# Kernel optimization log

Measured on AMD Instinct MI355X. Metric: run time of the kernel, lower is better.

Reference implementation:

```python
import jax, jax.numpy as jnp
import numpy as np

N_NODES = 50000
N_EDGES = 800000
NUM_FEATURES = 96
HIDDEN = 96


def _glorot(key, fan_in, fan_out):
    s = np.sqrt(6.0 / (fan_in + fan_out)).astype(np.float32)
    return jax.random.uniform(key, (fan_in, fan_out), minval=-s, maxval=s, dtype=jnp.float32)


def setup_inputs() -> dict:
    key = jax.random.key(0)
    ks = jax.random.split(key, 8)
    x = jax.random.normal(ks[0], (N_NODES, NUM_FEATURES), dtype=jnp.float32)
    edge_index = jax.random.randint(ks[1], (2, N_EDGES), 0, N_NODES, dtype=jnp.int64)
    return {
        "x": x,
        "W1": _glorot(ks[2], NUM_FEATURES, HIDDEN),
        "b1": jnp.zeros((HIDDEN,), jnp.float32),
        "W2": _glorot(ks[3], HIDDEN, HIDDEN),
        "b2": jnp.zeros((HIDDEN,), jnp.float32),
        "W3": _glorot(ks[4], HIDDEN, HIDDEN),
        "b3": jnp.zeros((HIDDEN,), jnp.float32),
        "edge_index": edge_index,
    }


def _gcn_conv(x, src, dst, W, b):
    """PyG GCNConv: add self-loops, symmetric normalization D^-1/2 (A+I) D^-1/2 X W + b."""
    n = x.shape[0]
    h = x @ W  # [N, H]
    # degree with self-loops (in-degree over dst, +1 for the self-loop)
    deg = jax.ops.segment_sum(jnp.ones_like(dst, dtype=h.dtype), dst, num_segments=n) + 1.0
    dinv = jax.lax.rsqrt(deg)  # [N]
    norm = dinv[src] * dinv[dst]  # [E]
    # scatter normalized messages; self-loop contributes h_i / deg_i
    agg = jax.ops.segment_sum(h[src] * norm[:, None], dst, num_segments=n)
    return agg + h * (dinv * dinv)[:, None] + b


def reference(x, W1, b1, W2, b2, W3, b3, edge_index):
    src, dst = edge_index[0], edge_index[1]
    # dropout is a no-op in eval mode (F.dropout with training=False)
    h = jax.nn.relu(_gcn_conv(x, src, dst, W1, b1))
    h = jax.nn.relu(_gcn_conv(h, src, dst, W2, b2))
    return _gcn_conv(h, src, dst, W3, b3)
```

## Files before the change

### kernel.cpp

```cpp
#include <hip/hip_runtime.h>

#define F 96
#define SCAN_B 1024
#define CHUNKS 8
#define CW 12
#define EWIN 2048

#define WT_IDX(c, k) ((c) * 96 + (((k) ^ (((c) & 7) << 2))))


__global__ void k_zero_i(int* __restrict__ p, int n) {
    int i = blockIdx.x * blockDim.x + threadIdx.x;
    if (i < n) p[i] = 0;
}

__global__ void k_hist(const int* __restrict__ dst, int* __restrict__ hist, int E) {
    int e = blockIdx.x * blockDim.x + threadIdx.x;
    if (e < E) atomicAdd(&hist[dst[e]], 1);
}

__global__ void k_dinv(const int* __restrict__ hist, float* __restrict__ dinv, int N) {
    int i = blockIdx.x * blockDim.x + threadIdx.x;
    if (i < N) dinv[i] = rsqrtf((float)hist[i] + 1.0f);
}

__global__ __launch_bounds__(SCAN_B) void k_scan1(const int* __restrict__ hist,
                                                  int* __restrict__ incl,
                                                  int* __restrict__ bsum, int N) {
    __shared__ int s[SCAN_B];
    int i = blockIdx.x * SCAN_B + threadIdx.x;
    int v = (i < N) ? hist[i] : 0;
    s[threadIdx.x] = v;
    __syncthreads();
    for (int off = 1; off < SCAN_B; off <<= 1) {
        int add = (threadIdx.x >= off) ? s[threadIdx.x - off] : 0;
        __syncthreads();
        s[threadIdx.x] += add;
        __syncthreads();
    }
    if (i < N) incl[i] = s[threadIdx.x];
    if (threadIdx.x == SCAN_B - 1) bsum[blockIdx.x] = s[SCAN_B - 1];
}

__global__ __launch_bounds__(SCAN_B) void k_scan2(int* __restrict__ bsum, int nb) {
    __shared__ int s[SCAN_B];
    int v = (threadIdx.x < nb) ? bsum[threadIdx.x] : 0;
    s[threadIdx.x] = v;
    __syncthreads();
    for (int off = 1; off < SCAN_B; off <<= 1) {
        int add = (threadIdx.x >= off) ? s[threadIdx.x - off] : 0;
        __syncthreads();
        s[threadIdx.x] += add;
        __syncthreads();
    }
    if (threadIdx.x < nb) bsum[threadIdx.x] = s[threadIdx.x] - v;
}

__global__ void k_scan3(const int* __restrict__ incl, const int* __restrict__ hist,
                        const int* __restrict__ bsum, int* __restrict__ row_ptr,
                        int* __restrict__ cursor, int N, int E) {
    int i = blockIdx.x * blockDim.x + threadIdx.x;
    if (i < N) {
        int start = incl[i] - hist[i] + bsum[i / SCAN_B];
        row_ptr[i] = start;
        cursor[i] = start;
    }
    if (i == 0) row_ptr[N] = E;
}

__global__ void k_place(const int* __restrict__ src, const int* __restrict__ dst,
                        int* __restrict__ cursor, int* __restrict__ csr_src, int E) {
    int e = blockIdx.x * blockDim.x + threadIdx.x;
    if (e >= E) return;
    int pos = atomicAdd(&cursor[dst[e]], 1);
    csr_src[pos] = src[e];
}


template <bool RELU_IN, bool CHIN_CHUNK, bool COUT_SCALED>
__global__ __launch_bounds__(256) void k_dense(const float* __restrict__ X,
                                               const float* __restrict__ W,
                                               float* __restrict__ H,
                                               const float* __restrict__ dinv,
                                               int N, int sIn, int sOut) {
    __shared__ float Wt[96 * 96];
    __shared__ float XsOs[64][100];
    int t = threadIdx.x;
    const size_t NCin = (size_t)N * sIn;
    const size_t NCout = (size_t)N * sOut;

    for (int i = t; i < F * F; i += 256) {
        int k = i / F, c = i % F;
        Wt[WT_IDX(c, k)] = W[i];
    }
    int row0 = blockIdx.x * 64;

    if (CHIN_CHUNK) {
        for (int q = t; q < 1536; q += 256) {
            int f = q / 192, rem = q % 192;
            int node = rem / 3, o = (rem % 3) * 4;
            int gr = row0 + node;
            float4 v = make_float4(0.f, 0.f, 0.f, 0.f);
            if (gr < N) {
                v = *reinterpret_cast<const float4*>(X + (size_t)f * NCin + (size_t)gr * sIn + o);
                if (RELU_IN) {
                    v.x = fmaxf(v.x, 0.f); v.y = fmaxf(v.y, 0.f);
                    v.z = fmaxf(v.z, 0.f); v.w = fmaxf(v.w, 0.f);
                }
            }
            *reinterpret_cast<float4*>(&XsOs[node][f * CW + o]) = v;
        }
    } else {
        for (int q = t; q < 1536; q += 256) {
            int node = q / 24, o = (q % 24) * 4;
            int gr = row0 + node;
            float4 v = make_float4(0.f, 0.f, 0.f, 0.f);
            if (gr < N) {
                v = *reinterpret_cast<const float4*>(X + (size_t)gr * F + o);
                if (RELU_IN) {
                    v.x = fmaxf(v.x, 0.f); v.y = fmaxf(v.y, 0.f);
                    v.z = fmaxf(v.z, 0.f); v.w = fmaxf(v.w, 0.f);
                }
            }
            *reinterpret_cast<float4*>(&XsOs[node][o]) = v;
        }
    }
    __syncthreads();

    int c2 = t & 31;
    int rg = t >> 5;
    float acc[8][3];
#pragma unroll
    for (int j = 0; j < 8; ++j) { acc[j][0] = 0.f; acc[j][1] = 0.f; acc[j][2] = 0.f; }

    for (int k4 = 0; k4 < F; k4 += 4) {
        float4 w0 = *reinterpret_cast<const float4*>(&Wt[WT_IDX(c2, k4)]);
        float4 w1 = *reinterpret_cast<const float4*>(&Wt[WT_IDX(c2 + 32, k4)]);
        float4 w2 = *reinterpret_cast<const float4*>(&Wt[WT_IDX(c2 + 64, k4)]);
#pragma unroll
        for (int j = 0; j < 8; ++j) {
            float4 xv = *reinterpret_cast<const float4*>(&XsOs[rg + 8 * j][k4]);
            acc[j][0] = fmaf(xv.x, w0.x, acc[j][0]);
            acc[j][1] = fmaf(xv.x, w1.x, acc[j][1]);
            acc[j][2] = fmaf(xv.x, w2.x, acc[j][2]);
            acc[j][0] = fmaf(xv.y, w0.y, acc[j][0]);
            acc[j][1] = fmaf(xv.y, w1.y, acc[j][1]);
            acc[j][2] = fmaf(xv.y, w2.y, acc[j][2]);
            acc[j][0] = fmaf(xv.z, w0.z, acc[j][0]);
            acc[j][1] = fmaf(xv.z, w1.z, acc[j][1]);
            acc[j][2] = fmaf(xv.z, w2.z, acc[j][2]);
            acc[j][0] = fmaf(xv.w, w0.w, acc[j][0]);
            acc[j][1] = fmaf(xv.w, w1.w, acc[j][1]);
            acc[j][2] = fmaf(xv.w, w2.w, acc[j][2]);
        }
    }
    __syncthreads();

#pragma unroll
    for (int j = 0; j < 8; ++j) {
        float dd = 1.f;
        if (COUT_SCALED) {
            int gr = row0 + rg + 8 * j;
            dd = (gr < N) ? dinv[gr] : 0.f;
        }
        XsOs[rg + 8 * j][c2]      = acc[j][0] * dd;
        XsOs[rg + 8 * j][c2 + 32] = acc[j][1] * dd;
        XsOs[rg + 8 * j][c2 + 64] = acc[j][2] * dd;
    }
    __syncthreads();

    if (COUT_SCALED) {
        int nfq = sOut >> 2;
        for (int q = t; q < 512 * nfq; q += 256) {
            int ch = q / (64 * nfq);
            int rem = q % (64 * nfq);
            int node = rem / nfq;
            int o4 = (rem % nfq) * 4;
            int gr = row0 + node;
            if (gr < N) {
                float4 v = make_float4(0.f, 0.f, 0.f, 0.f);
                if (o4 < CW) v = *reinterpret_cast<const float4*>(&XsOs[node][ch * CW + o4]);
                *reinterpret_cast<float4*>(H + (size_t)ch * NCout + (size_t)gr * sOut + o4) = v;
            }
        }
    } else {
        for (int q = t; q < 1536; q += 256) {
            int node = q / 24, o = (q % 24) * 4;
            int gr = row0 + node;
            if (gr < N) {
                *reinterpret_cast<float4*>(H + (size_t)gr * F + o) =
                    *reinterpret_cast<const float4*>(&XsOs[node][o]);
            }
        }
    }
}


template <bool OUT_ROW>
__global__ __launch_bounds__(256) void k_gather(const float* __restrict__ Hc,
                                                const int* __restrict__ csr_src,
                                                const int* __restrict__ row_ptr,
                                                const float* __restrict__ dinv,
                                                const float* __restrict__ bias,
                                                float* __restrict__ O,
                                                int N, int sA, int sB) {
    __shared__ int eidx[EWIN];
    const int tid = threadIdx.x;
    const int chunk = blockIdx.x & (CHUNKS - 1);
    const int nb0 = (blockIdx.x >> 3) * 16;
    const int slot = tid >> 4;
    const int f = tid & 15;
    const int node = nb0 + slot;
    const float* Hk = Hc + (size_t)chunk * (size_t)N * sA;

    float bf = (f < CW) ? bias[chunk * CW + f] : 0.f;
    const int nEnd = min(nb0 + 16, N);
    const int B0 = row_ptr[nb0];
    const int B1 = row_ptr[nEnd];
    int s0 = 0, s1 = 0;
    if (node < N) { s0 = row_ptr[node]; s1 = row_ptr[node + 1]; }

    float acc0 = 0.f, acc1 = 0.f;
    for (int wb = B0; wb < B1; wb += EWIN) {
        int wcnt = min(EWIN, B1 - wb);
        __syncthreads();
        for (int q = tid; q < wcnt; q += 256)
            eidx[q] = __builtin_nontemporal_load(csr_src + wb + q);
        __syncthreads();
        int e  = max(s0, wb);
        int e1 = min(s1, wb + wcnt);
        for (; e + 1 < e1; e += 2) {
            int i0 = eidx[e - wb];
            int i1 = eidx[e - wb + 1];
            acc0 += Hk[(size_t)i0 * sA + f];
            acc1 += Hk[(size_t)i1 * sA + f];
        }
        if (e < e1) acc0 += Hk[(size_t)eidx[e - wb] * sA + f];
    }
    if (node >= N) return;

    float di = dinv[node];
    float self = Hk[(size_t)node * sA + f];
    float r = fmaf(acc0 + acc1 + self, di, bf);

    if (OUT_ROW) {
        if (f < CW) O[(size_t)node * F + chunk * CW + f] = r;
    } else if (sB == 16) {
        O[(size_t)chunk * (size_t)N * 16 + (size_t)node * 16 + f] = r;
    } else {
        if (f < CW) O[(size_t)chunk * (size_t)N * CW + (size_t)node * CW + f] = r;
    }
}


__global__ void k_init_deg(float* __restrict__ deg, int N) {
    int i = blockIdx.x * blockDim.x + threadIdx.x;
    if (i < N) deg[i] = 1.0f;
}
__global__ void k_count(const int* __restrict__ dst, float* __restrict__ deg, int E) {
    int e = blockIdx.x * blockDim.x + threadIdx.x;
    if (e < E) atomicAdd(&deg[dst[e]], 1.0f);
}
__global__ void k_rsqrt(float* __restrict__ deg, int N) {
    int i = blockIdx.x * blockDim.x + threadIdx.x;
    if (i < N) deg[i] = rsqrtf(deg[i]);
}
__global__ void k_init_out(const float* __restrict__ H, const float* __restrict__ dinv,
                           const float* __restrict__ b, float* __restrict__ O, int N) {
    int idx = blockIdx.x * blockDim.x + threadIdx.x;
    if (idx >= N * F) return;
    int i = idx / F, f = idx % F;
    float di = dinv[i];
    O[idx] = fmaf(H[idx], di * di, b[f]);
}
__global__ __launch_bounds__(256) void k_scatter(const float* __restrict__ H,
                                                 const int* __restrict__ src,
                                                 const int* __restrict__ dst,
                                                 const float* __restrict__ dinv,
                                                 float* __restrict__ O, int E) {
    int t = blockIdx.x * 256 + threadIdx.x;
    int e = t >> 5;
    if (e >= E) return;
    int lf = t & 31;
    int s = src[e], d = dst[e];
    float nrm = dinv[s] * dinv[d];
    const float* hs = H + (size_t)s * F;
    float* od = O + (size_t)d * F;
#pragma unroll
    for (int j = 0; j < 3; ++j) atomicAdd(&od[lf + 32 * j], hs[lf + 32 * j] * nrm);
}


static inline size_t align64f(size_t x) { return (x + 63) & ~(size_t)63; }

extern "C" void kernel_launch(void* const* d_in, const int* in_sizes, int n_in,
                              void* d_out, int out_size, void* d_ws, size_t ws_size,
                              hipStream_t stream) {
    const float* x  = (const float*)d_in[0];
    const float* W1 = (const float*)d_in[1];
    const float* b1 = (const float*)d_in[2];
    const float* W2 = (const float*)d_in[3];
    const float* b2 = (const float*)d_in[4];
    const float* W3 = (const float*)d_in[5];
    const float* b3 = (const float*)d_in[6];
    const int*   ei = (const int*)d_in[7];

    const int N = in_sizes[0] / F;
    const int E = in_sizes[7] / 2;
    const int* src = ei;
    const int* dst = ei + E;
    const size_t NF = (size_t)N * F;

    const int thr = 256;
    dim3 blk(thr);
    int gN  = (N + thr - 1) / thr;
    int gE  = (E + thr - 1) / thr;
    int gDen = (N + 63) / 64;
    int gGat = CHUNKS * ((N + 15) / 16);
    int nScanB = (N + SCAN_B - 1) / SCAN_B;

    size_t o_rp  = align64f(N);
    size_t o_csr = o_rp + align64f((size_t)N + 1);
    size_t o_A   = o_csr + align64f((size_t)E + 4);
    size_t szA16 = (size_t)CHUNKS * N * 16 + 64;
    size_t szA12 = (size_t)CHUNKS * N * 12 + 64;
    size_t t1616 = (o_A + align64f(szA16) + szA16) * 4;
    size_t t1612 = (o_A + align64f(szA16) + szA12) * 4;
    size_t t1212 = (o_A + align64f(szA12) + szA12) * 4;

    int sA = 16, sB = 16;
    size_t o_B;
    bool csr_ok = (nScanB <= SCAN_B);
    if (ws_size >= t1616)      { sA = 16; sB = 16; o_B = o_A + align64f(szA16); }
    else if (ws_size >= t1612) { sA = 16; sB = 12; o_B = o_A + align64f(szA16); }
    else if (ws_size >= t1212) { sA = 12; sB = 12; o_B = o_A + align64f(szA12); }
    else csr_ok = false;

    float* wsf     = (float*)d_ws;
    float* dinv    = wsf;
    int*   row_ptr = (int*)(wsf + o_rp);
    int*   csr_src = (int*)(wsf + o_csr);
    float* A       = wsf + (csr_ok ? o_A : 0);
    float* B       = wsf + (csr_ok ? o_B : 0);
    int* hist   = (int*)A;
    int* incl   = hist + N;
    int* cursor = (int*)B;
    int* bsum   = cursor + N;

    float* out = (float*)d_out;

    if (csr_ok) {
        k_zero_i<<<gN, blk, 0, stream>>>(hist, N);
        k_hist<<<gE, blk, 0, stream>>>(dst, hist, E);
        k_scan1<<<nScanB, dim3(SCAN_B), 0, stream>>>(hist, incl, bsum, N);
        k_scan2<<<1, dim3(SCAN_B), 0, stream>>>(bsum, nScanB);
        k_scan3<<<gN, blk, 0, stream>>>(incl, hist, bsum, row_ptr, cursor, N, E);
        k_dinv<<<gN, blk, 0, stream>>>(hist, dinv, N);
        k_place<<<gE, blk, 0, stream>>>(src, dst, cursor, csr_src, E);

        k_dense<false, false, true><<<gDen, blk, 0, stream>>>(x, W1, A, dinv, N, F, sA);
        k_gather<false><<<gGat, blk, 0, stream>>>(A, csr_src, row_ptr, dinv, b1, B, N, sA, sB);
        k_dense<true, true, true><<<gDen, blk, 0, stream>>>(B, W2, A, dinv, N, sB, sA);
        k_gather<false><<<gGat, blk, 0, stream>>>(A, csr_src, row_ptr, dinv, b2, B, N, sA, sB);
        k_dense<true, true, true><<<gDen, blk, 0, stream>>>(B, W3, A, dinv, N, sB, sA);
        k_gather<true><<<gGat, blk, 0, stream>>>(A, csr_src, row_ptr, dinv, b3, out, N, sA, 0);
    } else {
        float* fdinv = (float*)d_ws;
        float* fA = fdinv + N;
        float* fB = fA + NF;
        int gNF = (int)((NF + thr - 1) / thr);
        int gSc = (int)(((size_t)E * 32 + thr - 1) / thr);
        k_init_deg<<<gN, blk, 0, stream>>>(fdinv, N);
        k_count<<<gE, blk, 0, stream>>>(dst, fdinv, E);
        k_rsqrt<<<gN, blk, 0, stream>>>(fdinv, N);
        k_dense<false, false, false><<<gDen, blk, 0, stream>>>(x, W1, fA, fdinv, N, F, F);
        k_init_out<<<gNF, blk, 0, stream>>>(fA, fdinv, b1, fB, N);
        k_scatter<<<gSc, blk, 0, stream>>>(fA, src, dst, fdinv, fB, E);
        k_dense<true, false, false><<<gDen, blk, 0, stream>>>(fB, W2, fA, fdinv, N, F, F);
        k_init_out<<<gNF, blk, 0, stream>>>(fA, fdinv, b2, out, N);
        k_scatter<<<gSc, blk, 0, stream>>>(fA, src, dst, fdinv, out, E);
        k_dense<true, false, false><<<gDen, blk, 0, stream>>>(out, W3, fA, fdinv, N, F, F);
        k_init_out<<<gNF, blk, 0, stream>>>(fA, fdinv, b3, fB, N);
        k_scatter<<<gSc, blk, 0, stream>>>(fA, src, dst, fdinv, fB, E);
        hipMemcpyAsync(out, fB, NF * sizeof(float), hipMemcpyDeviceToDevice, stream);
    }
}
```

Measured before the change: 444.9 us.

## Add float4 gather kernel with degree-sorted node slots for 16-stride chunks

```diff
diff --git a/kernel.cpp b/kernel.cpp
--- a/kernel.cpp
+++ b/kernel.cpp
@@ -197,6 +197,98 @@
 
 
 template <bool OUT_ROW>
+__global__ __launch_bounds__(256) void k_gather16(const float* __restrict__ Hc,
+                                                  const int* __restrict__ csr_src,
+                                                  const int* __restrict__ row_ptr,
+                                                  const float* __restrict__ dinv,
+                                                  const float* __restrict__ bias,
+                                                  float* __restrict__ O,
+                                                  int N, int sB) {
+    __shared__ int eidx[EWIN];
+    __shared__ int sdeg[64];
+    __shared__ int ord[64];
+    const int tid = threadIdx.x;
+    const int chunk = blockIdx.x & (CHUNKS - 1);
+    const int nb0 = (blockIdx.x >> 3) * 64;
+    const float* Hk = Hc + (size_t)chunk * (size_t)N * 16;
+
+    const int nEnd = min(nb0 + 64, N);
+    const int nloc = nEnd - nb0;
+
+    if (tid < 64) {
+        int nd = nb0 + tid;
+        sdeg[tid] = (nd < N) ? (row_ptr[nd + 1] - row_ptr[nd]) : -1;
+    }
+    __syncthreads();
+    if (tid < 64) {
+        int d = sdeg[tid];
+        int r = 0;
+#pragma unroll 8
+        for (int j = 0; j < 64; ++j) {
+            int dj = sdeg[j];
+            r += (dj < d) || (dj == d && j < tid);
+        }
+        ord[r] = tid;
+    }
+    __syncthreads();
+
+    const int slot = tid >> 2;
+    const int fl = (tid & 3) * 4;
+    int node = -1, s0 = 0, s1 = 0;
+    {
+        int on = ord[slot];
+        int nd = nb0 + on;
+        if (on < nloc && nd < N) { node = nd; s0 = row_ptr[nd]; s1 = row_ptr[nd + 1]; }
+    }
+
+    float4 a0 = make_float4(0.f, 0.f, 0.f, 0.f);
+    float4 a1 = make_float4(0.f, 0.f, 0.f, 0.f);
+    const int B0 = row_ptr[nb0];
+    const int B1 = row_ptr[nEnd];
+    for (int wb = B0; wb < B1; wb += EWIN) {
+        int wcnt = min(EWIN, B1 - wb);
+        __syncthreads();
+        for (int q = tid; q < wcnt; q += 256)
+            eidx[q] = __builtin_nontemporal_load(csr_src + wb + q);
+        __syncthreads();
+        int e  = max(s0, wb);
+        int e1 = min(s1, wb + wcnt);
+        for (; e + 1 < e1; e += 2) {
+            int i0 = eidx[e - wb];
+            int i1 = eidx[e - wb + 1];
+            float4 v0 = *reinterpret_cast<const float4*>(Hk + (size_t)i0 * 16 + fl);
+            float4 v1 = *reinterpret_cast<const float4*>(Hk + (size_t)i1 * 16 + fl);
+            a0.x += v0.x; a0.y += v0.y; a0.z += v0.z; a0.w += v0.w;
+            a1.x += v1.x; a1.y += v1.y; a1.z += v1.z; a1.w += v1.w;
+        }
+        if (e < e1) {
+            int i0 = eidx[e - wb];
+            float4 v0 = *reinterpret_cast<const float4*>(Hk + (size_t)i0 * 16 + fl);
+            a0.x += v0.x; a0.y += v0.y; a0.z += v0.z; a0.w += v0.w;
+        }
+    }
+    if (node < 0) return;
+
+    float di = dinv[node];
+    float4 self = *reinterpret_cast<const float4*>(Hk + (size_t)node * 16 + fl);
+    float4 b4 = make_float4(0.f, 0.f, 0.f, 0.f);
+    if (fl < CW) b4 = *reinterpret_cast<const float4*>(bias + chunk * CW + fl);
+    float4 r;
+    r.x = fmaf(a0.x + a1.x + self.x, di, b4.x);
+    r.y = fmaf(a0.y + a1.y + self.y, di, b4.y);
+    r.z = fmaf(a0.z + a1.z + self.z, di, b4.z);
+    r.w = fmaf(a0.w + a1.w + self.w, di, b4.w);
+
+    if (OUT_ROW) {
+        if (fl < CW)
+            *reinterpret_cast<float4*>(O + (size_t)node * F + chunk * CW + fl) = r;
+    } else {
+        *reinterpret_cast<float4*>(O + (size_t)chunk * (size_t)N * 16 + (size_t)node * 16 + fl) = r;
+    }
+}
+
+
+template <bool OUT_ROW>
 __global__ __launch_bounds__(256) void k_gather(const float* __restrict__ Hc,
                                                 const int* __restrict__ csr_src,
                                                 const int* __restrict__ row_ptr,
@@ -316,7 +408,8 @@
     int gN  = (N + thr - 1) / thr;
     int gE  = (E + thr - 1) / thr;
     int gDen = (N + 63) / 64;
-    int gGat = CHUNKS * ((N + 15) / 16);
+    int gGat16 = CHUNKS * ((N + 63) / 64);
+    int gGatLeg = CHUNKS * ((N + 15) / 16);
     int nScanB = (N + SCAN_B - 1) / SCAN_B;
 
     size_t o_rp  = align64f(N);
@@ -329,9 +422,10 @@
     size_t t1212 = (o_A + align64f(szA12) + szA12) * 4;
 
     int sA = 16, sB = 16;
-    size_t o_B;
+    size_t o_B = 0;
     bool csr_ok = (nScanB <= SCAN_B);
-    if (ws_size >= t1616)      { sA = 16; sB = 16; o_B = o_A + align64f(szA16); }
+    bool fast16 = false;
+    if (ws_size >= t1616)      { sA = 16; sB = 16; o_B = o_A + align64f(szA16); fast16 = true; }
     else if (ws_size >= t1612) { sA = 16; sB = 12; o_B = o_A + align64f(szA16); }
     else if (ws_size >= t1212) { sA = 12; sB = 12; o_B = o_A + align64f(szA12); }
     else csr_ok = false;
@@ -358,12 +452,21 @@
         k_dinv<<<gN, blk, 0, stream>>>(hist, dinv, N);
         k_place<<<gE, blk, 0, stream>>>(src, dst, cursor, csr_src, E);
 
-        k_dense<false, false, true><<<gDen, blk, 0, stream>>>(x, W1, A, dinv, N, F, sA);
-        k_gather<false><<<gGat, blk, 0, stream>>>(A, csr_src, row_ptr, dinv, b1, B, N, sA, sB);
-        k_dense<true, true, true><<<gDen, blk, 0, stream>>>(B, W2, A, dinv, N, sB, sA);
-        k_gather<false><<<gGat, blk, 0, stream>>>(A, csr_src, row_ptr, dinv, b2, B, N, sA, sB);
-        k_dense<true, true, true><<<gDen, blk, 0, stream>>>(B, W3, A, dinv, N, sB, sA);
-        k_gather<true><<<gGat, blk, 0, stream>>>(A, csr_src, row_ptr, dinv, b3, out, N, sA, 0);
+        if (fast16) {
+            k_dense<false, false, true><<<gDen, blk, 0, stream>>>(x, W1, A, dinv, N, F, 16);
+            k_gather16<false><<<gGat16, blk, 0, stream>>>(A, csr_src, row_ptr, dinv, b1, B, N, 16);
+            k_dense<true, true, true><<<gDen, blk, 0, stream>>>(B, W2, A, dinv, N, 16, 16);
+            k_gather16<false><<<gGat16, blk, 0, stream>>>(A, csr_src, row_ptr, dinv, b2, B, N, 16);
+            k_dense<true, true, true><<<gDen, blk, 0, stream>>>(B, W3, A, dinv, N, 16, 16);
+            k_gather16<true><<<gGat16, blk, 0, stream>>>(A, csr_src, row_ptr, dinv, b3, out, N, 0);
+        } else {
+            k_dense<false, false, true><<<gDen, blk, 0, stream>>>(x, W1, A, dinv, N, F, sA);
+            k_gather<false><<<gGatLeg, blk, 0, stream>>>(A, csr_src, row_ptr, dinv, b1, B, N, sA, sB);
+            k_dense<true, true, true><<<gDen, blk, 0, stream>>>(B, W2, A, dinv, N, sB, sA);
+            k_gather<false><<<gGatLeg, blk, 0, stream>>>(A, csr_src, row_ptr, dinv, b2, B, N, sA, sB);
+            k_dense<true, true, true><<<gDen, blk, 0, stream>>>(B, W3, A, dinv, N, sB, sA);
+            k_gather<true><<<gGatLeg, blk, 0, stream>>>(A, csr_src, row_ptr, dinv, b3, out, N, sA, 0);
+        }
     } else {
         float* fdinv = (float*)d_ws;
         float* fA = fdinv + N;
```

Result: faster. 404.7 us (-9.0%).
